# Performance work log

Measured on AMD Instinct MI355X. Metric: run time of the kernel, lower is better.

The kernel has to match this reference:

```python
import jax, jax.numpy as jnp
import numpy as np

DIM = 1024
NUM_HEADS = 16
HEAD_DIM = DIM // NUM_HEADS
SCALE = HEAD_DIM ** -0.5


def setup_inputs() -> dict:
    key = jax.random.key(0)
    k1, k2, k3 = jax.random.split(key, 3)
    B, N = 2, 2048
    x = jax.random.normal(k1, (B, N, DIM), dtype=jnp.float32)
    # qkv: Linear(dim, 3*dim, bias=False); proj: Linear(dim, dim) with bias
    w_qkv = jax.random.normal(k2, (3 * DIM, DIM), dtype=jnp.float32) * (DIM ** -0.5)
    w_proj = jax.random.normal(k3, (DIM, DIM), dtype=jnp.float32) * (DIM ** -0.5)
    b_proj = jnp.zeros((DIM,), dtype=jnp.float32)
    return {"x": x, "w_qkv": w_qkv, "w_proj": w_proj, "b_proj": b_proj}


def reference(x, w_qkv, w_proj, b_proj):
    B, N, C = x.shape
    H, D = NUM_HEADS, HEAD_DIM
    qkv = jnp.einsum('bnc,fc->bnf', x, w_qkv)                 # [B,N,3C]
    qkv = qkv.reshape(B, N, 3, H, D).transpose(2, 0, 3, 1, 4)  # [3,B,H,N,D]
    q, k, v = qkv[0], qkv[1], qkv[2]
    q = q * SCALE
    attn = jnp.einsum('bhnd,bhmd->bhnm', q, k)                 # [B,H,N,N]
    attn = jax.nn.softmax(attn, axis=-1)
    out = jnp.einsum('bhnm,bhmd->bhnd', attn, v)               # [B,H,N,D]
    out = out.transpose(0, 2, 1, 3).reshape(B, N, C)
    out = jnp.einsum('bnc,fc->bnf', out, w_proj) + b_proj
    return out
```

## Files before the change

kernel.cpp:

```cpp
#include <hip/hip_runtime.h>
#include <hip/hip_bf16.h>
#include <stdint.h>

typedef __attribute__((ext_vector_type(4))) float f32x4;
typedef __attribute__((ext_vector_type(16))) float f32x16;
typedef __attribute__((ext_vector_type(8))) short bf16x8;
typedef __attribute__((ext_vector_type(4))) short bf16x4;
typedef unsigned short ushort_t;

#define QSCALE 0.18033688f

__device__ inline short f2bf(float f) {
  unsigned u = __builtin_bit_cast(unsigned, f);
  u += 0x7fffu + ((u >> 16) & 1u);
  return (short)(u >> 16);
}

__device__ inline void gload_lds16(const void* g, void* l) {
  __builtin_amdgcn_global_load_lds(
      (const __attribute__((address_space(1))) void*)g,
      (__attribute__((address_space(3))) void*)l, 16, 0, 0);
}

__device__ inline unsigned cvtpk(float a, float b) {
  unsigned r;
  asm("v_cvt_pk_bf16_f32 %0, %1, %2" : "=v"(r) : "v"(a), "v"(b));
  return r;
}

__device__ inline void swap32u(unsigned& a, unsigned& b) {
  asm("v_permlane32_swap_b32 %0, %1" : "+v"(a), "+v"(b));
}

__global__ __launch_bounds__(256) void cvt_all(const float* __restrict__ x,
                                               const float* __restrict__ wq,
                                               const float* __restrict__ wp,
                                               short* __restrict__ Xb,
                                               short* __restrict__ Wq,
                                               short* __restrict__ Wp) {
  for (int i = blockIdx.x * 256 + threadIdx.x; i < 1048576; i += 2048 * 256) {
    const float* s;
    short* d;
    int off;
    if (i < 524288)       { s = x;  d = Xb; off = i; }
    else if (i < 917504)  { s = wq; d = Wq; off = i - 524288; }
    else                  { s = wp; d = Wp; off = i - 917504; }
    const float4* sv = (const float4*)s;
    float4 a = sv[2 * off], b = sv[2 * off + 1];
    bf16x8 o;
    o[0] = f2bf(a.x); o[1] = f2bf(a.y); o[2] = f2bf(a.z); o[3] = f2bf(a.w);
    o[4] = f2bf(b.x); o[5] = f2bf(b.y); o[6] = f2bf(b.z); o[7] = f2bf(b.w);
    ((bf16x8*)d)[off] = o;
  }
}

template <int F32OUT, int SPLITV, int BXPX>
__global__ __launch_bounds__(256, 2) void gemm_db(const short* __restrict__ A,
                                                  const short* __restrict__ B,
                                                  void* __restrict__ Cv,
                                                  short* __restrict__ Vtg,
                                                  const float* __restrict__ bias,
                                                  int scale_cols, float scale_val,
                                                  int M, int N, int K) {
  __shared__ char smem[65536];
  short* Ab0 = (short*)smem;
  short* Bb0 = (short*)(smem + 32768);
  const int tid = threadIdx.x, wv = tid >> 6, ln = tid & 63;
  const int wm = wv >> 1, wn = wv & 1;
  const int id = blockIdx.x;
  const int xcd = id & 7, local = id >> 3;
  const int bx = xcd * BXPX + local % BXPX;
  const int by = local / BXPX;
  const int bn0 = bx * 128, bm0 = by * 128;
  const int nt = K >> 6;

  const int srow = ln >> 3;
  const int scol = ((ln & 7) ^ (ln >> 3)) * 8;
  const int fln = ln & 15;
  const int fk = ln >> 4;

  f32x4 acc[4][4] = {};

  auto stage = [&](int t, int s) {
    const size_t k0 = (size_t)t << 6;
#pragma unroll
    for (int rd = 0; rd < 4; rd++) {
      const int ch = 4 * wv + rd;
      gload_lds16(A + (size_t)(bm0 + ch * 8 + srow) * K + k0 + scol,
                  (char*)(Ab0 + s * 8192) + ch * 1024);
      gload_lds16(B + (size_t)(bn0 + ch * 8 + srow) * K + k0 + scol,
                  (char*)(Bb0 + s * 8192) + ch * 1024);
    }
  };

  stage(0, 0);
  stage(1, 1);
  asm volatile("s_waitcnt vmcnt(8)" ::: "memory");
  __builtin_amdgcn_s_barrier();
  __builtin_amdgcn_sched_barrier(0);

  for (int t = 0; t < nt; t++) {
    const int s = t & 1;
    const char* Ap = (const char*)(Ab0 + s * 8192);
    const char* Bp = (const char*)(Bb0 + s * 8192);

    bf16x8 af[4][2], bf[4][2];
#pragma unroll
    for (int m = 0; m < 4; m++) {
      const int R = wm * 64 + m * 16 + fln;
#pragma unroll
      for (int kk = 0; kk < 2; kk++)
        af[m][kk] = *(const bf16x8*)(Ap + R * 128 + ((((kk << 2) | fk) ^ (R & 7)) << 4));
    }
#pragma unroll
    for (int n = 0; n < 4; n++) {
      const int R = wn * 64 + n * 16 + fln;
#pragma unroll
      for (int kk = 0; kk < 2; kk++)
        bf[n][kk] = *(const bf16x8*)(Bp + R * 128 + ((((kk << 2) | fk) ^ (R & 7)) << 4));
    }

    __builtin_amdgcn_s_setprio(1);
#pragma unroll
    for (int kk = 0; kk < 2; kk++)
#pragma unroll
      for (int m = 0; m < 4; m++)
#pragma unroll
        for (int n = 0; n < 4; n++)
          acc[m][n] = __builtin_amdgcn_mfma_f32_16x16x32_bf16(af[m][kk], bf[n][kk], acc[m][n], 0, 0, 0);
    __builtin_amdgcn_s_setprio(0);

    if (t + 1 < nt) {
      __builtin_amdgcn_s_barrier();
      if (t + 2 < nt) {
        stage(t + 2, s);
        asm volatile("s_waitcnt vmcnt(8)" ::: "memory");
      } else {
        asm volatile("s_waitcnt vmcnt(0)" ::: "memory");
      }
      __builtin_amdgcn_s_barrier();
      __builtin_amdgcn_sched_barrier(0);
    }
  }

  if constexpr (SPLITV) {
    if (bn0 >= 2048) {
      __syncthreads();
      short* Vl = (short*)smem;
#pragma unroll
      for (int m = 0; m < 4; m++) {
        const int tok0 = wm * 64 + m * 16 + fk * 4;
#pragma unroll
        for (int n = 0; n < 4; n++) {
          const int f_loc = wn * 64 + n * 16 + fln;
          bf16x4 w;
#pragma unroll
          for (int j = 0; j < 4; j++) w[j] = f2bf(acc[m][n][j]);
          *(bf16x4*)(Vl + f_loc * 136 + tok0) = w;
        }
      }
      __syncthreads();
      const int fbase = bn0 - 2048, bb = bm0 >> 11, ntok0 = bm0 & 2047;
#pragma unroll
      for (int pass = 0; pass < 8; pass++) {
        const int f_loc = wv * 32 + pass * 4 + (ln >> 4);
        const int f = fbase + f_loc;
        const int g = (bb * 16 + (f >> 6)) * 64 + (f & 63);
        bf16x8 w = *(const bf16x8*)(Vl + f_loc * 136 + (ln & 15) * 8);
        *(bf16x8*)(Vtg + (size_t)g * 2048 + ntok0 + (ln & 15) * 8) = w;
      }
      return;
    }
  }

  const int r0 = bm0 + wm * 64, c0 = bn0 + wn * 64;
  const int fg4 = fk * 4;
#pragma unroll
  for (int m = 0; m < 4; m++) {
    const int row0 = r0 + m * 16 + fg4;
#pragma unroll
    for (int n = 0; n < 4; n++) {
      const int col = c0 + n * 16 + fln;
      if constexpr (SPLITV) {
        const float sc = (col < scale_cols) ? scale_val : 1.0f;
#pragma unroll
        for (int j = 0; j < 4; j++)
          ((short*)Cv)[(size_t)(row0 + j) * 2048 + col] = f2bf(acc[m][n][j] * sc);
      } else {
#pragma unroll
        for (int j = 0; j < 4; j++) {
          float v = acc[m][n][j];
          if (col < scale_cols) v *= scale_val;
          if (F32OUT) ((float*)Cv)[(size_t)(row0 + j) * N + col] = v + bias[col];
          else        ((short*)Cv)[(size_t)(row0 + j) * N + col] = f2bf(v);
        }
      }
    }
  }
}

__global__ __launch_bounds__(256, 2) void attn_fwd(const short* __restrict__ QK,
                                                   const short* __restrict__ Vtg,
                                                   short* __restrict__ AO) {
  __shared__ short Ks[3][64 * 64];
  __shared__ short Vt[3][64 * 64];
  const int tid = threadIdx.x, wv = tid >> 6, ln = tid & 63;
  const int lq = ln & 31, hi = ln >> 5;
  const int id = blockIdx.x;
  const int c = (id & 7) * 64 + (id >> 3);
  const int qt = c & 15, bh = c >> 4;
  const int b = bh >> 4, h = bh & 15;
  const short* base = QK + (size_t)(b * 2048) * 2048 + h * 64;
  const short* Kg = base + 1024;
  const short* Vg = Vtg + (size_t)bh * 64 * 2048;
  const int qrow = qt * 128 + wv * 32 + lq;

  bf16x8 qf[4];
  {
    const short* Qrow = base + (size_t)qrow * 2048;
#pragma unroll
    for (int ds = 0; ds < 4; ds++)
      qf[ds] = *(const bf16x8*)(Qrow + ds * 16 + hi * 8);
  }

  const int krow = ln >> 3;
  const int kcol = ((ln & 7) ^ (ln >> 3)) * 8;

  float l_run = 0.f;
  f32x16 o0 = {}, o1 = {};

#define STAGE(t, s)                                                              \
  {                                                                              \
    _Pragma("unroll")                                                            \
    for (int rd = 0; rd < 2; rd++) {                                             \
      const int r8 = 16 * wv + 8 * rd + krow;                                    \
      gload_lds16(Kg + (size_t)((t) * 64 + r8) * 2048 + kcol,                    \
                  (char*)Ks[s] + (2 * wv + rd) * 1024);                          \
      gload_lds16(Vg + (size_t)r8 * 2048 + (t) * 64 + kcol,                      \
                  (char*)Vt[s] + (2 * wv + rd) * 1024);                          \
    }                                                                            \
  }

  STAGE(0, 0);
  STAGE(1, 1);

  for (int t = 0; t < 32; t++) {
    const int s = t % 3;
    if (t < 31) asm volatile("s_waitcnt vmcnt(4)" ::: "memory");
    else        asm volatile("s_waitcnt vmcnt(0)" ::: "memory");
    __builtin_amdgcn_s_barrier();
    __builtin_amdgcn_sched_barrier(0);
    if (t + 2 < 32) STAGE(t + 2, (t + 2) % 3);

    f32x16 c0 = {}, c1 = {};
    const char* Kb = (const char*)Ks[s];
    __builtin_amdgcn_s_setprio(1);
#pragma unroll
    for (int ds = 0; ds < 4; ds++) {
      const int cp = (ds * 2 + hi) ^ (lq & 7);
      bf16x8 ka0 = *(const bf16x8*)(Kb + lq * 128 + cp * 16);
      bf16x8 ka1 = *(const bf16x8*)(Kb + (32 + lq) * 128 + cp * 16);
      c0 = __builtin_amdgcn_mfma_f32_32x32x16_bf16(ka0, qf[ds], c0, 0, 0, 0);
      c1 = __builtin_amdgcn_mfma_f32_32x32x16_bf16(ka1, qf[ds], c1, 0, 0, 0);
    }
    __builtin_amdgcn_s_setprio(0);

#pragma unroll
    for (int r = 0; r < 16; r++) c0[r] = __builtin_amdgcn_exp2f(c0[r]);
#pragma unroll
    for (int r = 0; r < 16; r++) c1[r] = __builtin_amdgcn_exp2f(c1[r]);
    {
      float st[8];
#pragma unroll
      for (int r = 0; r < 8; r++)
        st[r] = (c0[2 * r] + c0[2 * r + 1]) + (c1[2 * r] + c1[2 * r + 1]);
#pragma unroll
      for (int r = 0; r < 4; r++) st[r] += st[r + 4];
      l_run += (st[0] + st[1]) + (st[2] + st[3]);
    }

    bf16x8 pa[4];
#pragma unroll
    for (int cs = 0; cs < 2; cs++) {
      const f32x16& p = cs ? c1 : c0;
#pragma unroll
      for (int ksl = 0; ksl < 2; ksl++) {
        unsigned A0 = cvtpk(p[8 * ksl + 0], p[8 * ksl + 1]);
        unsigned A1 = cvtpk(p[8 * ksl + 2], p[8 * ksl + 3]);
        unsigned B0 = cvtpk(p[8 * ksl + 4], p[8 * ksl + 5]);
        unsigned B1 = cvtpk(p[8 * ksl + 6], p[8 * ksl + 7]);
        swap32u(A0, B0);
        swap32u(A1, B1);
        union { unsigned u[4]; bf16x8 v; } tmp;
        tmp.u[0] = A0; tmp.u[1] = A1; tmp.u[2] = B0; tmp.u[3] = B1;
        pa[cs * 2 + ksl] = tmp.v;
      }
    }

    const char* Vb = (const char*)Vt[s];
    __builtin_amdgcn_s_setprio(1);
#pragma unroll
    for (int ks = 0; ks < 4; ks++) {
      const int cp = (ks * 2 + hi) ^ (lq & 7);
      bf16x8 va0 = *(const bf16x8*)(Vb + lq * 128 + cp * 16);
      bf16x8 va1 = *(const bf16x8*)(Vb + (32 + lq) * 128 + cp * 16);
      o0 = __builtin_amdgcn_mfma_f32_32x32x16_bf16(va0, pa[ks], o0, 0, 0, 0);
      o1 = __builtin_amdgcn_mfma_f32_32x32x16_bf16(va1, pa[ks], o1, 0, 0, 0);
    }
    __builtin_amdgcn_s_setprio(0);
  }
#undef STAGE

  l_run += __shfl_xor(l_run, 32);
  const float inv = __builtin_amdgcn_rcpf(l_run);
  short* Arow = AO + ((size_t)(b * 2048) + qrow) * 1024 + h * 64;
#pragma unroll
  for (int dt = 0; dt < 2; dt++) {
    const f32x16& o = dt ? o1 : o0;
#pragma unroll
    for (int g = 0; g < 4; g++) {
      bf16x4 w;
#pragma unroll
      for (int i = 0; i < 4; i++) w[i] = f2bf(o[4 * g + i] * inv);
      *(bf16x4*)(Arow + dt * 32 + 8 * g + 4 * hi) = w;
    }
  }
}

extern "C" void kernel_launch(void* const* d_in, const int* in_sizes, int n_in,
                              void* d_out, int out_size, void* d_ws, size_t ws_size,
                              hipStream_t stream) {
  const float* x = (const float*)d_in[0];
  const float* w_qkv = (const float*)d_in[1];
  const float* w_proj = (const float*)d_in[2];
  const float* b_proj = (const float*)d_in[3];
  float* out = (float*)d_out;

  char* ws = (char*)d_ws;
  short* Xb  = (short*)(ws + 0);
  short* Wq  = (short*)(ws + 8388608);
  short* Wp  = (short*)(ws + 14680064);
  short* QK  = (short*)(ws + 16777216);
  short* Vtg = (short*)(ws + 33554432);
  short* AO  = (short*)(ws + 41943040);

  cvt_all<<<2048, 256, 0, stream>>>(x, w_qkv, w_proj, Xb, Wq, Wp);

  gemm_db<0, 1, 3><<<dim3(768), 256, 0, stream>>>(Xb, Wq, QK, Vtg, nullptr,
                                                  1024, QSCALE, 4096, 3072, 1024);

  attn_fwd<<<dim3(512), 256, 0, stream>>>(QK, Vtg, AO);

  gemm_db<1, 0, 1><<<dim3(256), 256, 0, stream>>>(AO, Wp, out, nullptr, b_proj,
                                                  0, 1.0f, 4096, 1024, 1024);
}
```

Baseline: 102.9 us.

## Replace QKV GEMM with 256x256-tile 8-wave kernel using phased ping-pong pipeline

Adds a dedicated QKV projection kernel with 256x256 output tiles, 8 waves per block and 192 blocks. Each K-step is split into four phases that interleave LDS fragment reads, asynchronous global-to-LDS loads for the next step, and MFMA bursts. The goal is more operand reuse per byte loaded and better overlap of memory with compute. The V-transpose epilogue now writes bf16x4 strided stores straight to global instead of going through an LDS transpose, which may give less coalesced writes. 192 blocks on a 256-CU part also leaves some CUs idle.

```diff
diff --git a/kernel.cpp b/kernel.cpp
--- a/kernel.cpp
+++ b/kernel.cpp
@@ -54,13 +54,115 @@
   }
 }
 
-template <int F32OUT, int SPLITV, int BXPX>
+__global__ __launch_bounds__(512, 2) void gemm8p(const short* __restrict__ A,
+                                                 const short* __restrict__ B,
+                                                 short* __restrict__ QK,
+                                                 short* __restrict__ Vtg) {
+  __shared__ short lds[65536];
+  const int tid = threadIdx.x, wv = tid >> 6, ln = tid & 63;
+  const int wm = wv >> 2, wn = wv & 3;
+  const int id = blockIdx.x;
+  const int flat = (id & 7) * 24 + (id >> 3);
+  const int bn0 = (flat >> 4) * 256, bm0 = (flat & 15) * 256;
+  const int K = 1024, nt = 16;
+
+  const int fln = ln & 15, fk = ln >> 4;
+  const int sR = ln >> 2;
+  const int schunk = (ln & 3) ^ ((ln >> 2) & 3);
+
+  f32x4 acc[8][4] = {};
+
+  auto stage_half = [&](int t, int which) {
+    const int par = t & 1;
+    const int kh = which >> 1;
+    const bool isB = which & 1;
+    const short* src = isB ? B : A;
+    const int base0 = isB ? bn0 : bm0;
+    short* dst = lds + (isB ? 32768 : 0) + par * 16384 + kh * 8192;
+#pragma unroll
+    for (int r = 0; r < 2; r++) {
+      const int R = (wv * 2 + r) * 16 + sR;
+      gload_lds16(src + (size_t)(base0 + R) * K + t * 64 + kh * 32 + schunk * 8,
+                  (char*)(dst + (wv * 2 + r) * 512));
+    }
+  };
+  auto rdA = [&](int par, int kh, int mr) -> bf16x8 {
+    const int R = wm * 128 + mr * 16 + fln;
+    return *(const bf16x8*)(lds + par * 16384 + kh * 8192 + R * 32 + ((fk ^ (R & 3)) << 3));
+  };
+  auto rdB = [&](int par, int kh, int nr) -> bf16x8 {
+    const int R = wn * 64 + nr * 16 + fln;
+    return *(const bf16x8*)(lds + 32768 + par * 16384 + kh * 8192 + R * 32 + ((fk ^ (R & 3)) << 3));
+  };
+
+  stage_half(0, 0); stage_half(0, 1); stage_half(0, 2); stage_half(0, 3);
+  asm volatile("s_waitcnt vmcnt(4)" ::: "memory");
+  __builtin_amdgcn_s_barrier();
+  __builtin_amdgcn_sched_barrier(0);
+
+  bf16x8 bfr[4];
+  for (int t = 0; t < nt; t++) {
+    const int par = t & 1;
+#pragma unroll
+    for (int ph = 0; ph < 4; ph++) {
+      const int kh = ph >> 1;
+      const int mbase = (ph & 1) * 4;
+      bf16x8 af[4];
+#pragma unroll
+      for (int i = 0; i < 4; i++) af[i] = rdA(par, kh, mbase + i);
+      if ((ph & 1) == 0) {
+#pragma unroll
+        for (int n = 0; n < 4; n++) bfr[n] = rdB(par, kh, n);
+      }
+      if (t + 1 < nt) stage_half(t + 1, ph);
+      __builtin_amdgcn_s_barrier();
+      __builtin_amdgcn_sched_barrier(0);
+      __builtin_amdgcn_s_setprio(1);
+#pragma unroll
+      for (int i = 0; i < 4; i++)
+#pragma unroll
+        for (int n = 0; n < 4; n++)
+          acc[mbase + i][n] =
+              __builtin_amdgcn_mfma_f32_16x16x32_bf16(af[i], bfr[n], acc[mbase + i][n], 0, 0, 0);
+      __builtin_amdgcn_s_setprio(0);
+      if (ph & 1) {
+        if (t + 1 < nt) asm volatile("s_waitcnt vmcnt(4)" ::: "memory");
+        else            asm volatile("s_waitcnt vmcnt(0)" ::: "memory");
+      }
+      __builtin_amdgcn_s_barrier();
+      __builtin_amdgcn_sched_barrier(0);
+    }
+  }
+
+  const int r0 = bm0 + wm * 128, c0base = bn0 + wn * 64;
+#pragma unroll
+  for (int mr = 0; mr < 8; mr++) {
+    const int row0 = r0 + mr * 16 + fk * 4;
+#pragma unroll
+    for (int nr = 0; nr < 4; nr++) {
+      const int col = c0base + nr * 16 + fln;
+      if (col < 2048) {
+        const float sc = (col < 1024) ? QSCALE : 1.0f;
+#pragma unroll
+        for (int j = 0; j < 4; j++)
+          QK[(size_t)(row0 + j) * 2048 + col] = f2bf(acc[mr][nr][j] * sc);
+      } else {
+        const int f = col - 2048, h = f >> 6, d = f & 63;
+        const int bb = row0 >> 11, ntok = row0 & 2047;
+        bf16x4 w;
+#pragma unroll
+        for (int j = 0; j < 4; j++) w[j] = f2bf(acc[mr][nr][j]);
+        *(bf16x4*)(Vtg + ((size_t)((bb * 16 + h) * 64 + d)) * 2048 + ntok) = w;
+      }
+    }
+  }
+}
+
+template <int BXPX>
 __global__ __launch_bounds__(256, 2) void gemm_db(const short* __restrict__ A,
                                                   const short* __restrict__ B,
-                                                  void* __restrict__ Cv,
-                                                  short* __restrict__ Vtg,
+                                                  float* __restrict__ Cv,
                                                   const float* __restrict__ bias,
-                                                  int scale_cols, float scale_val,
                                                   int M, int N, int K) {
   __shared__ char smem[65536];
   short* Ab0 = (short*)smem;
@@ -143,36 +245,6 @@
     }
   }
 
-  if constexpr (SPLITV) {
-    if (bn0 >= 2048) {
-      __syncthreads();
-      short* Vl = (short*)smem;
-#pragma unroll
-      for (int m = 0; m < 4; m++) {
-        const int tok0 = wm * 64 + m * 16 + fk * 4;
-#pragma unroll
-        for (int n = 0; n < 4; n++) {
-          const int f_loc = wn * 64 + n * 16 + fln;
-          bf16x4 w;
-#pragma unroll
-          for (int j = 0; j < 4; j++) w[j] = f2bf(acc[m][n][j]);
-          *(bf16x4*)(Vl + f_loc * 136 + tok0) = w;
-        }
-      }
-      __syncthreads();
-      const int fbase = bn0 - 2048, bb = bm0 >> 11, ntok0 = bm0 & 2047;
-#pragma unroll
-      for (int pass = 0; pass < 8; pass++) {
-        const int f_loc = wv * 32 + pass * 4 + (ln >> 4);
-        const int f = fbase + f_loc;
-        const int g = (bb * 16 + (f >> 6)) * 64 + (f & 63);
-        bf16x8 w = *(const bf16x8*)(Vl + f_loc * 136 + (ln & 15) * 8);
-        *(bf16x8*)(Vtg + (size_t)g * 2048 + ntok0 + (ln & 15) * 8) = w;
-      }
-      return;
-    }
-  }
-
   const int r0 = bm0 + wm * 64, c0 = bn0 + wn * 64;
   const int fg4 = fk * 4;
 #pragma unroll
@@ -181,20 +253,9 @@
 #pragma unroll
     for (int n = 0; n < 4; n++) {
       const int col = c0 + n * 16 + fln;
-      if constexpr (SPLITV) {
-        const float sc = (col < scale_cols) ? scale_val : 1.0f;
-#pragma unroll
-        for (int j = 0; j < 4; j++)
-          ((short*)Cv)[(size_t)(row0 + j) * 2048 + col] = f2bf(acc[m][n][j] * sc);
-      } else {
-#pragma unroll
-        for (int j = 0; j < 4; j++) {
-          float v = acc[m][n][j];
-          if (col < scale_cols) v *= scale_val;
-          if (F32OUT) ((float*)Cv)[(size_t)(row0 + j) * N + col] = v + bias[col];
-          else        ((short*)Cv)[(size_t)(row0 + j) * N + col] = f2bf(v);
-        }
-      }
+#pragma unroll
+      for (int j = 0; j < 4; j++)
+        Cv[(size_t)(row0 + j) * N + col] = acc[m][n][j] + bias[col];
     }
   }
 }
@@ -346,11 +407,9 @@
 
   cvt_all<<<2048, 256, 0, stream>>>(x, w_qkv, w_proj, Xb, Wq, Wp);
 
-  gemm_db<0, 1, 3><<<dim3(768), 256, 0, stream>>>(Xb, Wq, QK, Vtg, nullptr,
-                                                  1024, QSCALE, 4096, 3072, 1024);
+  gemm8p<<<dim3(192), 512, 0, stream>>>(Xb, Wq, QK, Vtg);
 
   attn_fwd<<<dim3(512), 256, 0, stream>>>(QK, Vtg, AO);
 
-  gemm_db<1, 0, 1><<<dim3(256), 256, 0, stream>>>(AO, Wp, out, nullptr, b_proj,
-                                                  0, 1.0f, 4096, 1024, 1024);
-}
+  gemm_db<1><<<dim3(256), 256, 0, stream>>>(AO, Wp, out, b_proj, 4096, 1024, 1024);
+}
```

Measured after the change: 109.9 us. +6.8%, slower.
